# Performance work log

Hardware: AMD Instinct MI355X
Metric: run time of the kernel (lower is better)

Reference implementation:

```python
import jax, jax.numpy as jnp
import numpy as np

R = 3.9
EPS = 0.3
BETA = 0.15
STEPS = 15


def setup_inputs() -> dict:
    key = jax.random.key(0)
    k1, k2 = jax.random.split(key)
    drive = jax.random.uniform(k1, (2048, 1, 16384), dtype=jnp.float32)
    K = jnp.abs(jax.random.uniform(k2, (3,), dtype=jnp.float32))
    K = K / K.sum()
    return {"drive": drive, "K": K}


def reference(drive, K):
    # Circular 3-tap conv: torch conv1d is cross-correlation, padded circularly,
    # so local[i] = K[0]*m[i-1] + K[1]*m[i] + K[2]*m[i+1] (indices mod L).
    def step(grid, _):
        mapped = R * grid * (1.0 - grid)
        local = (K[0] * jnp.roll(mapped, 1, axis=-1)
                 + K[1] * mapped
                 + K[2] * jnp.roll(mapped, -1, axis=-1))
        physics = (1.0 - EPS) * mapped + EPS * local
        grid = (1.0 - BETA) * physics + BETA * drive
        return grid, None

    grid, _ = jax.lax.scan(step, drive, None, length=STEPS)
    return jnp.clip(grid, 0.0001, 1.0 - 0.0001)
```

## Files before the change

### kernel.cpp

```cpp
#include <hip/hip_runtime.h>


constexpr float Rc    = 3.9f;
constexpr float EPSc  = 0.3f;
constexpr float BETAc = 0.15f;
constexpr int   STEPS = 15;
constexpr int   L     = 16384;
constexpr int   T     = 1024;
constexpr int   C     = L / T;

__global__ __launch_bounds__(1024, 8)
void cml1d_kernel(const float* __restrict__ drive,
                  const float* __restrict__ K,
                  float* __restrict__ out) {
    __shared__ float sm_first[2][T];
    __shared__ float sm_last[2][T];

    const int t = threadIdx.x;
    const size_t base = (size_t)blockIdx.x * L + (size_t)t * C;
    const float4* __restrict__ d4 = reinterpret_cast<const float4*>(drive + base);
    float4* __restrict__ o4 = reinterpret_cast<float4*>(out + base);

    const float K0 = K[0], K1 = K[1], K2 = K[2];
    const float A  = (1.0f - BETAc) * (1.0f - EPSc);
    const float B  = (1.0f - BETAc) * EPSc;
    const float c0 = B * K0;
    const float c1 = A + B * K1;
    const float c2 = B * K2;

    float d[C], g[C];
    #pragma unroll
    for (int j = 0; j < C / 4; ++j) {
        float4 v = d4[j];
        d[4*j+0] = v.x; d[4*j+1] = v.y; d[4*j+2] = v.z; d[4*j+3] = v.w;
    }
    #pragma unroll
    for (int i = 0; i < C; ++i) g[i] = d[i];

    const int tl = (t == 0)     ? (T - 1) : (t - 1);
    const int tr = (t == T - 1) ? 0       : (t + 1);

    for (int s = 0; s < STEPS; ++s) {
        const int pb = s & 1;
        float t0 = Rc * g[0];
        float m0 = t0 - t0 * g[0];
        float t1 = Rc * g[C-1];
        float mlast = t1 - t1 * g[C-1];
        sm_first[pb][t] = m0;
        sm_last[pb][t]  = mlast;
        __syncthreads();
        float mprev = sm_last[pb][tl];
        float mrh   = sm_first[pb][tr];

        float mcur = m0;
        #pragma unroll
        for (int i = 0; i < C; ++i) {
            float mnext;
            if (i == C - 1)      mnext = mrh;
            else if (i == C - 2) mnext = mlast;
            else {
                float tt = Rc * g[i+1];
                mnext = tt - tt * g[i+1];
            }
            g[i] = c0 * mprev + (c1 * mcur + (c2 * mnext + BETAc * d[i]));
            mprev = mcur;
            mcur  = mnext;
        }
    }

    const float lo = (float)(0.0001);
    const float hi = (float)(1.0 - 0.0001);
    #pragma unroll
    for (int j = 0; j < C / 4; ++j) {
        float4 v;
        v.x = fminf(fmaxf(g[4*j+0], lo), hi);
        v.y = fminf(fmaxf(g[4*j+1], lo), hi);
        v.z = fminf(fmaxf(g[4*j+2], lo), hi);
        v.w = fminf(fmaxf(g[4*j+3], lo), hi);
        o4[j] = v;
    }
}

extern "C" void kernel_launch(void* const* d_in, const int* in_sizes, int n_in,
                              void* d_out, int out_size, void* d_ws, size_t ws_size,
                              hipStream_t stream) {
    const float* drive = (const float*)d_in[0];
    const float* K     = (const float*)d_in[1];
    float* out         = (float*)d_out;
    const int rows = in_sizes[0] / L;
    cml1d_kernel<<<dim3(rows), dim3(T), 0, stream>>>(drive, K, out);
}
```

Before: 245.3 us.

## Replace block-wide syncs with wave-local halo segments and lane shuffles

Each 64-lane wave now owns a 1024-cell segment of a row, with 32 redundant ghost cells on each side, so 17 cells per lane. Neighbour exchange between steps uses __shfl_up/__shfl_down instead of shared memory and __syncthreads. This removes the per-step block-wide barriers and shared-memory traffic of the 1024-thread blocks. In exchange it adds about 6% redundant compute and replaces float4 loads and stores with strided scalar accesses. The beta*drive term is also precomputed and the update is written as explicit fma calls.

```diff
diff --git a/kernel.cpp b/kernel.cpp
--- a/kernel.cpp
+++ b/kernel.cpp
@@ -6,20 +6,23 @@
 constexpr float BETAc = 0.15f;
 constexpr int   STEPS = 15;
 constexpr int   L     = 16384;
-constexpr int   T     = 1024;
-constexpr int   C     = L / T;
+constexpr int   CE    = 17;
+constexpr int   SEG   = 1024;
+constexpr int   GHOST = 32;
+constexpr int   TPB   = 256;
+constexpr int   SEGS_PER_ROW = L / SEG;
 
-__global__ __launch_bounds__(1024, 8)
+__global__ __launch_bounds__(TPB)
 void cml1d_kernel(const float* __restrict__ drive,
                   const float* __restrict__ K,
                   float* __restrict__ out) {
-    __shared__ float sm_first[2][T];
-    __shared__ float sm_last[2][T];
-
-    const int t = threadIdx.x;
-    const size_t base = (size_t)blockIdx.x * L + (size_t)t * C;
-    const float4* __restrict__ d4 = reinterpret_cast<const float4*>(drive + base);
-    float4* __restrict__ o4 = reinterpret_cast<float4*>(out + base);
+    const int lane  = threadIdx.x & 63;
+    const int wave  = threadIdx.x >> 6;
+    const int gwave = blockIdx.x * (TPB / 64) + wave;
+    const int row   = gwave >> 4;
+    const int seg   = gwave & (SEGS_PER_ROW - 1);
+    const size_t rowbase = (size_t)row * L;
+    const int cstart = seg * SEG - GHOST + lane * CE;
 
     const float K0 = K[0], K1 = K[1], K2 = K[2];
     const float A  = (1.0f - BETAc) * (1.0f - EPSc);
@@ -28,56 +31,49 @@
     const float c1 = A + B * K1;
     const float c2 = B * K2;
 
-    float d[C], g[C];
+    float g[CE], bd[CE];
     #pragma unroll
-    for (int j = 0; j < C / 4; ++j) {
-        float4 v = d4[j];
-        d[4*j+0] = v.x; d[4*j+1] = v.y; d[4*j+2] = v.z; d[4*j+3] = v.w;
+    for (int i = 0; i < CE; ++i) {
+        int idx = (cstart + i) & (L - 1);
+        float v = drive[rowbase + (size_t)idx];
+        g[i]  = v;
+        bd[i] = BETAc * v;
     }
-    #pragma unroll
-    for (int i = 0; i < C; ++i) g[i] = d[i];
-
-    const int tl = (t == 0)     ? (T - 1) : (t - 1);
-    const int tr = (t == T - 1) ? 0       : (t + 1);
 
     for (int s = 0; s < STEPS; ++s) {
-        const int pb = s & 1;
-        float t0 = Rc * g[0];
-        float m0 = t0 - t0 * g[0];
-        float t1 = Rc * g[C-1];
-        float mlast = t1 - t1 * g[C-1];
-        sm_first[pb][t] = m0;
-        sm_last[pb][t]  = mlast;
-        __syncthreads();
-        float mprev = sm_last[pb][tl];
-        float mrh   = sm_first[pb][tr];
+        float t0    = Rc * g[0];
+        float m0    = t0 - t0 * g[0];
+        float t1    = Rc * g[CE - 1];
+        float mlast = t1 - t1 * g[CE - 1];
+        float mleft  = __shfl_up(mlast, 1);
+        float mright = __shfl_down(m0, 1);
 
-        float mcur = m0;
+        float mprev = mleft;
+        float mcur  = m0;
         #pragma unroll
-        for (int i = 0; i < C; ++i) {
+        for (int i = 0; i < CE; ++i) {
             float mnext;
-            if (i == C - 1)      mnext = mrh;
-            else if (i == C - 2) mnext = mlast;
+            if (i == CE - 1)      mnext = mright;
+            else if (i == CE - 2) mnext = mlast;
             else {
-                float tt = Rc * g[i+1];
-                mnext = tt - tt * g[i+1];
+                float tt = Rc * g[i + 1];
+                mnext = tt - tt * g[i + 1];
             }
-            g[i] = c0 * mprev + (c1 * mcur + (c2 * mnext + BETAc * d[i]));
+            g[i] = fmaf(c0, mprev, fmaf(c1, mcur, fmaf(c2, mnext, bd[i])));
             mprev = mcur;
             mcur  = mnext;
         }
     }
 
-    const float lo = (float)(0.0001);
-    const float hi = (float)(1.0 - 0.0001);
+    const float lo = 0.0001f;
+    const float hi = 0.9999f;
     #pragma unroll
-    for (int j = 0; j < C / 4; ++j) {
-        float4 v;
-        v.x = fminf(fmaxf(g[4*j+0], lo), hi);
-        v.y = fminf(fmaxf(g[4*j+1], lo), hi);
-        v.z = fminf(fmaxf(g[4*j+2], lo), hi);
-        v.w = fminf(fmaxf(g[4*j+3], lo), hi);
-        o4[j] = v;
+    for (int i = 0; i < CE; ++i) {
+        int pos = lane * CE + i;
+        if (pos >= GHOST && pos < GHOST + SEG) {
+            int idx = (cstart + i) & (L - 1);
+            out[rowbase + (size_t)idx] = fminf(fmaxf(g[i], lo), hi);
+        }
     }
 }
 
@@ -87,6 +83,8 @@
     const float* drive = (const float*)d_in[0];
     const float* K     = (const float*)d_in[1];
     float* out         = (float*)d_out;
-    const int rows = in_sizes[0] / L;
-    cml1d_kernel<<<dim3(rows), dim3(T), 0, stream>>>(drive, K, out);
+    const int rows   = in_sizes[0] / L;
+    const int gwaves = rows * SEGS_PER_ROW;
+    const int blocks = gwaves / (TPB / 64);
+    cml1d_kernel<<<dim3(blocks), dim3(TPB), 0, stream>>>(drive, K, out);
 }
```

New measurement: 337.0 us. 37.4% more time.
